# Optimization experiments

Hardware: AMD Instinct MI355X
Metric: run time of the kernel (lower is better)

Reference implementation:

```python
import jax, jax.numpy as jnp
import numpy as np

VOCAB = 6; C_IN = 4; D = 256; L = 4; T = 4096; B = 2
EXPAND = 2; DI = EXPAND * D  # 512
DS = 16; DCONV = 4; DTR = 16  # dt_rank = ceil(D/16)


def setup_inputs() -> dict:
    key = jax.random.key(0)
    ks = jax.random.split(key, 16)
    rn = lambda k, shape, s=0.02: jax.random.normal(k, shape, jnp.float32) * s
    return {
        "seq": jax.random.randint(ks[0], (B, T), 0, VOCAB),
        "input": jax.random.normal(ks[1], (B, T, C_IN), jnp.float32),
        "emb_table": rn(ks[2], (VOCAB, D)),
        "inproj_w": rn(ks[3], (D, C_IN)),
        "inproj_b": jnp.zeros((D,), jnp.float32),
        "blk_in_w": rn(ks[4], (L, 2 * DI, D)),
        "blk_in_b": jnp.zeros((L, 2 * DI), jnp.float32),
        "conv_w": rn(ks[5], (L, DI, DCONV), 0.1),
        "conv_b": jnp.zeros((L, DI), jnp.float32),
        "xproj_w": rn(ks[6], (L, DTR + 2 * DS, DI)),
        "dt_w": rn(ks[7], (L, DI, DTR), 0.1),
        "dt_b": rn(ks[8], (L, DI), 0.1),
        "A_log": jnp.log(jnp.broadcast_to(jnp.arange(1, DS + 1, dtype=jnp.float32), (L, DI, DS))),
        "Dp": jnp.ones((L, DI), jnp.float32),
        "blk_out_w": rn(ks[9], (L, D, DI)),
        "blk_out_b": jnp.zeros((L, D), jnp.float32),
        "ln_g": jnp.ones((L, D), jnp.float32),
        "ln_b": jnp.zeros((L, D), jnp.float32),
        "head_w": rn(ks[10], (VOCAB, D)),
        "head_b": jnp.zeros((VOCAB,), jnp.float32),
        "outp_w": rn(ks[11], (C_IN, D)),
        "outp_b": jnp.zeros((C_IN,), jnp.float32),
    }


def _layernorm(x, g, b):
    mu = x.mean(-1, keepdims=True)
    var = ((x - mu) ** 2).mean(-1, keepdims=True)
    return (x - mu) * jax.lax.rsqrt(var + 1e-5) * g + b


def _mamba(x, in_w, in_b, cw, cb, xpw, dtw, dtb, alog, dparam, ow, ob):
    # x: (B, T, D). Standard mamba-ssm Mamba block (d_state=DS, d_conv=DCONV, expand=2).
    Bsz = x.shape[0]
    xz = x @ in_w.T + in_b                      # (B, T, 2*DI)
    xs, z = jnp.split(xz, 2, axis=-1)           # each (B, T, DI)
    # causal depthwise conv1d over time
    xt = jnp.pad(xs.transpose(0, 2, 1), ((0, 0), (0, 0), (DCONV - 1, 0)))  # (B, DI, T+3)
    xc = jax.lax.conv_general_dilated(xt, cw[:, None, :], (1,), 'VALID',
                                      feature_group_count=DI)             # (B, DI, T)
    xc = jax.nn.silu(xc + cb[None, :, None]).transpose(0, 2, 1)           # (B, T, DI)
    # input-dependent dt, B, C
    x_dbl = xc @ xpw.T                          # (B, T, DTR+2*DS)
    dt, Bm, Cm = jnp.split(x_dbl, [DTR, DTR + DS], axis=-1)
    dt = jax.nn.softplus(dt @ dtw.T + dtb)      # (B, T, DI)
    A = -jnp.exp(alog)                          # (DI, DS)
    dA = jnp.exp(dt[..., None] * A)                                  # (B, T, DI, DS)
    dBx = dt[..., None] * Bm[:, :, None, :] * xc[..., None]          # (B, T, DI, DS)

    def step(h, ins):
        dA_t, dBx_t, C_t = ins                  # (B,DI,DS), (B,DI,DS), (B,DS)
        h = dA_t * h + dBx_t
        return h, jnp.einsum('bds,bs->bd', h, C_t)

    h0 = jnp.zeros((Bsz, DI, DS), xc.dtype)
    _, ys = jax.lax.scan(step, h0, (dA.transpose(1, 0, 2, 3),
                                    dBx.transpose(1, 0, 2, 3),
                                    Cm.transpose(1, 0, 2)))
    y = ys.transpose(1, 0, 2) + dparam * xc     # (B, T, DI)
    y = y * jax.nn.silu(z)
    return y @ ow.T + ob                        # (B, T, D)


def reference(seq, input, emb_table, inproj_w, inproj_b, blk_in_w, blk_in_b,
              conv_w, conv_b, xproj_w, dt_w, dt_b, A_log, Dp,
              blk_out_w, blk_out_b, ln_g, ln_b, head_w, head_b, outp_w, outp_b):
    x = emb_table[seq] + input @ inproj_w.T + inproj_b   # (B, T, D)
    for l in range(L):
        mx = _mamba(x, blk_in_w[l], blk_in_b[l], conv_w[l], conv_b[l],
                    xproj_w[l], dt_w[l], dt_b[l], A_log[l], Dp[l],
                    blk_out_w[l], blk_out_b[l])
        x = _layernorm(x + mx, ln_g[l], ln_b[l])
    return (x @ head_w.T + head_b, x @ outp_w.T + outp_b)
```

## Files before the change

### kernel.cpp

```cpp
#include <hip/hip_runtime.h>

typedef unsigned short u16;
typedef unsigned int u32;
typedef short bf16x8 __attribute__((ext_vector_type(8)));
typedef float f32x4 __attribute__((ext_vector_type(4)));

#define Tlen 4096
#define NTOK 8192
#define NCH  128
#define CH   32

enum : int {
  OFF_EMB     = 16,
  OFF_INPUT   = OFF_EMB + 1536,
  OFF_INPROJW = OFF_INPUT + 32768,
  OFF_INPROJB = OFF_INPROJW + 1024,
  OFF_BLKINW  = OFF_INPROJB + 256,
  OFF_BLKINB  = OFF_BLKINW + 1048576,
  OFF_CONVW   = OFF_BLKINB + 4096,
  OFF_CONVB   = OFF_CONVW + 8192,
  OFF_XPROJW  = OFF_CONVB + 2048,
  OFF_DTW     = OFF_XPROJW + 98304,
  OFF_DTB     = OFF_DTW + 32768,
  OFF_A       = OFF_DTB + 2048,
  OFF_DP      = OFF_A + 32768,
  OFF_BLKOUTW = OFF_DP + 2048,
  OFF_BLKOUTB = OFF_BLKOUTW + 524288,
  OFF_LNG     = OFF_BLKOUTB + 1024,
  OFF_LNB     = OFF_LNG + 1024,
  OFF_HEADW   = OFF_LNB + 1024,
  OFF_HEADB   = OFF_HEADW + 1536,
  OFF_OUTPW   = OFF_HEADB + 16,
  OFF_OUTPB   = OFF_OUTPW + 1024,
  OFF_X       = OFF_OUTPB + 16,
  OFF_DT      = OFF_X + NTOK*256,
  OFF_SD      = OFF_DT + NTOK*512,
  OFF_BM      = OFF_SD + 131072,
  OFF_CM      = OFF_BM + 131072,
  OFF_XSBL    = OFF_CM + 131072,
  OFF_Z16     = OFF_XSBL + NTOK*256,
  OFF_XC16    = OFF_Z16 + NTOK*256,
  OFF_X16     = OFF_XC16 + NTOK*256,
  OFF_WIN16   = OFF_X16 + NTOK*128,
  OFF_WOUT16  = OFF_WIN16 + 524288,
  OFF_BXD16   = OFF_WOUT16 + 262144,
  OFF_T       = OFF_BXD16 + 49152,
  OFF_TOT     = OFF_T + 131072,
};

__device__ inline float bf2f(u16 u) { return __uint_as_float(((u32)u) << 16); }
__device__ inline u16 f2bf(float f) {
  u32 x = __float_as_uint(f);
  u32 r = x + 0x7fffu + ((x >> 16) & 1u);
  return (u16)(r >> 16);
}

__global__ void k_sentinel(u32* dout, int nw) {
  int i = blockIdx.x * blockDim.x + threadIdx.x;
  if (i < nw) dout[i] = 0x46404640u;
}

__global__ void k_detect(const u16* emb, int n, int* flag) {
  __shared__ int bad;
  if (threadIdx.x == 0) bad = 0;
  __syncthreads();
  int local = 0;
  for (int i = threadIdx.x; i < n; i += blockDim.x) {
    float v = bf2f(emb[i]);
    if (!(fabsf(v) < 100.0f)) local = 1;
  }
  if (local) atomicOr(&bad, 1);
  __syncthreads();
  if (threadIdx.x == 0) flag[0] = bad ? 0 : 1;
}

struct Seg { const void* src; int n; int off; int op; };
struct ConvArgs { Seg seg[21]; int nseg; };

__global__ void k_convert(ConvArgs a, float* ws, const int* flag) {
  int isb = *flag;
  for (int sgi = 0; sgi < a.nseg; sgi++) {
    Seg sg = a.seg[sgi];
    for (int i = blockIdx.x * blockDim.x + threadIdx.x; i < sg.n;
         i += gridDim.x * blockDim.x) {
      float v;
      if (isb) v = bf2f(((const u16*)sg.src)[i]);
      else     v = ((const float*)sg.src)[i];
      if (sg.op) v = -__expf(v);
      ws[sg.off + i] = v;
    }
  }
}

__global__ void k_w16(float* ws) {
  u16* win = (u16*)(ws + OFF_WIN16);
  u16* wout = (u16*)(ws + OFF_WOUT16);
  for (int i = blockIdx.x * blockDim.x + threadIdx.x; i < 1048576 + 524288;
       i += gridDim.x * blockDim.x) {
    if (i < 1048576) win[i] = f2bf(ws[OFF_BLKINW + i]);
    else             wout[i - 1048576] = f2bf(ws[OFF_BLKOUTW + i - 1048576]);
  }
}

__global__ void k_bxd(float* ws) {
  u16* bxd = (u16*)(ws + OFF_BXD16);
  const int NXD = 4 * 48 * 512;
  for (int idx = blockIdx.x * blockDim.x + threadIdx.x; idx < NXD;
       idx += gridDim.x * blockDim.x) {
    int l = idx / (48 * 512);
    int rem = idx - l * (48 * 512);
    int row = rem >> 9, k = rem & 511;
    const float* xpw = ws + OFF_XPROJW + l * 24576;
    float v = (row < 32) ? xpw[(16 + row) * 512 + k] : xpw[(row - 32) * 512 + k];
    bxd[idx] = f2bf(v);
  }
}

__global__ __launch_bounds__(256) void k_embed(const int* seq, float* ws) {
  int n = blockIdx.x, d = threadIdx.x;
  int s = seq[n];
  float4 iv = *(const float4*)(ws + OFF_INPUT + n * 4);
  float4 wv = *(const float4*)(ws + OFF_INPROJW + d * 4);
  float acc = ws[OFF_EMB + s * 256 + d] + ws[OFF_INPROJB + d]
            + iv.x * wv.x + iv.y * wv.y + iv.z * wv.z + iv.w * wv.w;
  ws[OFF_X + (size_t)n * 256 + d] = acc;
  ((u16*)(ws + OFF_X16))[(size_t)n * 256 + d] = f2bf(acc);
}

__global__ __launch_bounds__(256) void k_gemm_in(float* ws, int l) {
  __shared__ u16 As[128][40];
  __shared__ u16 Bs[128][40];
  __shared__ u16 ot[64][136];
  int m0 = blockIdx.x * 128, n0g = blockIdx.y * 128;
  int t = threadIdx.x;
  int w = t >> 6, lane = t & 63;
  int fr = lane & 15, fq = lane >> 4;
  int wr = (w >> 1) * 64, wc = (w & 1) * 64;
  const u16* Ab = (const u16*)(ws + OFF_X16);
  const u16* Bb = (const u16*)(ws + OFF_WIN16) + (size_t)l * 1024 * 256;
  const float* bias = ws + OFF_BLKINB + l * 1024;
  f32x4 acc[4][4] = {};
  for (int k0 = 0; k0 < 256; k0 += 32) {
    __syncthreads();
    #pragma unroll
    for (int cc = 0; cc < 2; cc++) {
      int c = t + cc * 256;
      int row = c >> 2, cg = (c & 3) * 8;
      *(uint4*)&As[row][cg] =
          *(const uint4*)(Ab + (size_t)(m0 + row) * 256 + k0 + cg);
      *(uint4*)&Bs[row][cg] =
          *(const uint4*)(Bb + (size_t)(n0g + row) * 256 + k0 + cg);
    }
    __syncthreads();
    bf16x8 af[4], bf_[4];
    #pragma unroll
    for (int f = 0; f < 4; f++) {
      af[f]  = *(const bf16x8*)&As[wr + f * 16 + fr][fq * 8];
      bf_[f] = *(const bf16x8*)&Bs[wc + f * 16 + fr][fq * 8];
    }
    #pragma unroll
    for (int i = 0; i < 4; i++)
      #pragma unroll
      for (int j = 0; j < 4; j++)
        acc[i][j] = __builtin_amdgcn_mfma_f32_16x16x32_bf16(af[i], bf_[j],
                                                            acc[i][j], 0, 0, 0);
  }
  u16* plane; int cb0;
  if (n0g < 512) { plane = (u16*)(ws + OFF_XSBL); cb0 = n0g; }
  else           { plane = (u16*)(ws + OFF_Z16);  cb0 = n0g - 512; }
  #pragma unroll
  for (int hh = 0; hh < 2; hh++) {
    __syncthreads();
    if ((w >> 1) == hh) {
      #pragma unroll
      for (int i = 0; i < 4; i++)
        #pragma unroll
        for (int j = 0; j < 4; j++) {
          int col = wc + j * 16 + fr;
          float bv = bias[n0g + col];
          #pragma unroll
          for (int r = 0; r < 4; r++)
            ot[i * 16 + fq * 4 + r][col] = f2bf(acc[i][j][r] + bv);
        }
    }
    __syncthreads();
    int row = t >> 2, c0 = (t & 3) * 32;
    uint4 q0 = *(const uint4*)&ot[row][c0];
    uint4 q1 = *(const uint4*)&ot[row][c0 + 8];
    uint4 q2 = *(const uint4*)&ot[row][c0 + 16];
    uint4 q3 = *(const uint4*)&ot[row][c0 + 24];
    u16* dst = plane + (size_t)(m0 + hh * 64 + row) * 512 + cb0 + c0;
    *(uint4*)(dst + 0) = q0;
    *(uint4*)(dst + 8) = q1;
    *(uint4*)(dst + 16) = q2;
    *(uint4*)(dst + 24) = q3;
  }
}

__global__ __launch_bounds__(512) void k_conv(float* ws, int l) {
  int n0 = blockIdx.x * 16;
  int d = threadIdx.x;
  const float* cw = ws + OFF_CONVW + l * 2048;
  float4 w4 = *(const float4*)(cw + d * 4);
  float cbv = ws[OFF_CONVB + l * 512 + d];
  const u16* xs16 = (const u16*)(ws + OFF_XSBL);
  u16* xc16 = (u16*)(ws + OFF_XC16);
  float xm3, xm2, xm1;
  if ((n0 & (Tlen - 1)) == 0) {
    xm3 = xm2 = xm1 = 0.f;
  } else {
    xm3 = bf2f(xs16[(size_t)(n0 - 3) * 512 + d]);
    xm2 = bf2f(xs16[(size_t)(n0 - 2) * 512 + d]);
    xm1 = bf2f(xs16[(size_t)(n0 - 1) * 512 + d]);
  }
  #pragma unroll
  for (int tok = 0; tok < 16; tok++) {
    int n = n0 + tok;
    float xc = bf2f(xs16[(size_t)n * 512 + d]);
    float acc = cbv + xm3 * w4.x + xm2 * w4.y + xm1 * w4.z + xc * w4.w;
    float sv = acc / (1.f + __expf(-acc));
    xc16[(size_t)n * 512 + d] = f2bf(sv);
    xm3 = xm2; xm2 = xm1; xm1 = xc;
  }
}

__global__ __launch_bounds__(256) void k_gemm_bct(float* ws, int l) {
  int m0 = blockIdx.x * 64;
  int w = threadIdx.x >> 6, lane = threadIdx.x & 63;
  const u16* Ab = (const u16*)(ws + OFF_XC16);
  const u16* Bb = (const u16*)(ws + OFF_BXD16) + (size_t)l * 48 * 512;
  int ak = (lane >> 4) * 8;
  const u16* ap = Ab + (size_t)(m0 + w * 16 + (lane & 15)) * 512 + ak;
  int rowbase = w * 16 + (lane >> 4) * 4;
  const u16* bp = Bb + (size_t)(lane & 15) * 512 + ak;
  f32x4 acc[3] = {};
  bf16x8 a0 = *(const bf16x8*)ap;
  bf16x8 b0[3];
  #pragma unroll
  for (int j = 0; j < 3; j++) b0[j] = *(const bf16x8*)(bp + (size_t)j * 8192);
  #pragma unroll 2
  for (int k0 = 1; k0 < 16; k0++) {
    bf16x8 a1 = *(const bf16x8*)(ap + k0 * 32);
    bf16x8 b1[3];
    #pragma unroll
    for (int j = 0; j < 3; j++)
      b1[j] = *(const bf16x8*)(bp + (size_t)j * 8192 + k0 * 32);
    #pragma unroll
    for (int j = 0; j < 3; j++)
      acc[j] = __builtin_amdgcn_mfma_f32_16x16x32_bf16(a0, b0[j], acc[j], 0, 0, 0);
    a0 = a1;
    #pragma unroll
    for (int j = 0; j < 3; j++) b0[j] = b1[j];
  }
  #pragma unroll
  for (int j = 0; j < 3; j++)
    acc[j] = __builtin_amdgcn_mfma_f32_16x16x32_bf16(a0, b0[j], acc[j], 0, 0, 0);
  int c = lane & 15;
  #pragma unroll
  for (int r = 0; r < 4; r++) {
    ws[OFF_BM + (size_t)(m0 + rowbase + r) * 16 + c] = acc[0][r];
    ws[OFF_CM + (size_t)(m0 + rowbase + r) * 16 + c] = acc[1][r];
    ws[OFF_T  + (size_t)(m0 + rowbase + r) * 16 + c] = acc[2][r];
  }
}

__global__ __launch_bounds__(256) void k_dtexp(float* ws, int l) {
  __shared__ float Ts[16][16];
  int n0 = blockIdx.x * 16;
  int t = threadIdx.x;
  Ts[t >> 4][t & 15] = ws[OFF_T + (size_t)n0 * 16 + t];
  const float* dtwp = ws + OFF_DTW + (size_t)l * 8192;
  float w0[16], w1[16];
  #pragma unroll
  for (int q = 0; q < 4; q++) {
    *(float4*)&w0[q * 4] = *(const float4*)(dtwp + (2 * t) * 16 + q * 4);
    *(float4*)&w1[q * 4] = *(const float4*)(dtwp + (2 * t + 1) * 16 + q * 4);
  }
  float b0 = ws[OFF_DTB + l * 512 + 2 * t];
  float b1 = ws[OFF_DTB + l * 512 + 2 * t + 1];
  __syncthreads();
  u16* dt16 = (u16*)(ws + OFF_DT);
  #pragma unroll
  for (int tok = 0; tok < 16; tok++) {
    float s0 = b0, s1 = b1;
    #pragma unroll
    for (int r = 0; r < 16; r++) {
      float tv = Ts[tok][r];
      s0 += tv * w0[r];
      s1 += tv * w1[r];
    }
    float d0 = (s0 > 20.f) ? s0 : log1pf(__expf(s0));
    float d1 = (s1 > 20.f) ? s1 : log1pf(__expf(s1));
    *(u32*)(dt16 + (size_t)(n0 + tok) * 512 + 2 * t) =
        (u32)f2bf(d0) | ((u32)f2bf(d1) << 16);
  }
}

__global__ __launch_bounds__(512) void k_scan1(float* ws, int l) {
  __shared__ u16 dt_s[8][512];
  __shared__ u16 xc_s[8][512];
  __shared__ float Bls[CH * 16];
  int blk = blockIdx.x;
  int b = blk >> 7, ch = blk & 127;
  int d = threadIdx.x;
  int nbase = b * Tlen + ch * CH;
  Bls[d] = ws[OFF_BM + (size_t)nbase * 16 + d];
  const float* Ap = ws + OFF_A + l * 8192 + d * 16;
  float Ar[16];
  *(float4*)&Ar[0]  = *(const float4*)(Ap + 0);
  *(float4*)&Ar[4]  = *(const float4*)(Ap + 4);
  *(float4*)&Ar[8]  = *(const float4*)(Ap + 8);
  *(float4*)&Ar[12] = *(const float4*)(Ap + 12);
  float h[16];
  #pragma unroll
  for (int s = 0; s < 16; s++) h[s] = 0.f;
  float sumdt = 0.f;
  const u16* dtg = (const u16*)(ws + OFF_DT) + (size_t)nbase * 512;
  const u16* xcg = (const u16*)(ws + OFF_XC16) + (size_t)nbase * 512;
  int lr = d >> 6, lc = (d & 63) * 8;
  uint4 pd = *(const uint4*)(dtg + (size_t)lr * 512 + lc);
  uint4 px = *(const uint4*)(xcg + (size_t)lr * 512 + lc);
  for (int st = 0; st < 4; st++) {
    *(uint4*)&dt_s[lr][lc] = pd;
    *(uint4*)&xc_s[lr][lc] = px;
    if (st < 3) {
      pd = *(const uint4*)(dtg + (size_t)(st * 8 + 8 + lr) * 512 + lc);
      px = *(const uint4*)(xcg + (size_t)(st * 8 + 8 + lr) * 512 + lc);
    }
    __syncthreads();
    #pragma unroll
    for (int tk = 0; tk < 8; tk++) {
      int tt = st * 8 + tk;
      float dtv = bf2f(dt_s[tk][d]);
      float xv = bf2f(xc_s[tk][d]);
      sumdt += dtv;
      float dtx = dtv * xv;
      #pragma unroll
      for (int s = 0; s < 16; s++)
        h[s] = __expf(dtv * Ar[s]) * h[s] + dtx * Bls[tt * 16 + s];
    }
    __syncthreads();
  }
  ws[OFF_SD + (size_t)blk * 512 + d] = sumdt;
  float* bl = ws + OFF_XSBL + ((size_t)blk * 512 + d) * 16;
  *(float4*)(bl + 0)  = make_float4(h[0], h[1], h[2], h[3]);
  *(float4*)(bl + 4)  = make_float4(h[4], h[5], h[6], h[7]);
  *(float4*)(bl + 8)  = make_float4(h[8], h[9], h[10], h[11]);
  *(float4*)(bl + 12) = make_float4(h[12], h[13], h[14], h[15]);
}

__global__ __launch_bounds__(256) void k_scan2(float* ws, int l) {
  int q = blockIdx.x * 256 + threadIdx.x;
  int b = q >> 13, ds = q & 8191, d = ds >> 4;
  float Av = ws[OFF_A + l * 8192 + ds];
  float* blhs = ws + OFF_XSBL;
  const float* sdp = ws + OFF_SD;
  size_t base = (size_t)(b * NCH) * 8192 + ds;
  size_t sbase = (size_t)(b * NCH) * 512 + d;
  float blv[4], sd[4];
  #pragma unroll
  for (int k = 0; k < 4; k++) {
    blv[k] = blhs[base + (size_t)k * 8192];
    sd[k] = sdp[sbase + (size_t)k * 512];
  }
  float h = 0.f;
  for (int g = 0; g < 32; g++) {
    float nblv[4], nsd[4];
    if (g < 31) {
      #pragma unroll
      for (int k = 0; k < 4; k++) {
        nblv[k] = blhs[base + (size_t)(g * 4 + 4 + k) * 8192];
        nsd[k] = sdp[sbase + (size_t)(g * 4 + 4 + k) * 512];
      }
    }
    #pragma unroll
    for (int k = 0; k < 4; k++) {
      blhs[base + (size_t)(g * 4 + k) * 8192] = h;
      h = __expf(sd[k] * Av) * h + blv[k];
    }
    #pragma unroll
    for (int k = 0; k < 4; k++) { blv[k] = nblv[k]; sd[k] = nsd[k]; }
  }
}

__global__ __launch_bounds__(512) void k_scan3(float* ws, int l) {
  __shared__ u16 dt_s[8][512];
  __shared__ u16 xc_s[8][512];
  __shared__ u16 z_s[8][512];
  __shared__ u16 y_s[8][512];
  __shared__ float Bls[CH * 16];
  __shared__ float Cls[CH * 16];
  int blk = blockIdx.x;
  int b = blk >> 7, ch = blk & 127;
  int d = threadIdx.x;
  int nbase = b * Tlen + ch * CH;
  Bls[d] = ws[OFF_BM + (size_t)nbase * 16 + d];
  Cls[d] = ws[OFF_CM + (size_t)nbase * 16 + d];
  const float* Ap = ws + OFF_A + l * 8192 + d * 16;
  float Ar[16];
  *(float4*)&Ar[0]  = *(const float4*)(Ap + 0);
  *(float4*)&Ar[4]  = *(const float4*)(Ap + 4);
  *(float4*)&Ar[8]  = *(const float4*)(Ap + 8);
  *(float4*)&Ar[12] = *(const float4*)(Ap + 12);
  float Dv = ws[OFF_DP + l * 512 + d];
  const float* hs = ws + OFF_XSBL + ((size_t)blk * 512 + d) * 16;
  float h[16];
  *(float4*)&h[0]  = *(const float4*)(hs + 0);
  *(float4*)&h[4]  = *(const float4*)(hs + 4);
  *(float4*)&h[8]  = *(const float4*)(hs + 8);
  *(float4*)&h[12] = *(const float4*)(hs + 12);
  const u16* dtg = (const u16*)(ws + OFF_DT) + (size_t)nbase * 512;
  u16* xcg = (u16*)(ws + OFF_XC16) + (size_t)nbase * 512;
  const u16* zg = (const u16*)(ws + OFF_Z16) + (size_t)nbase * 512;
  int lr = d >> 6, lc = (d & 63) * 8;
  size_t off0 = (size_t)lr * 512 + lc;
  uint4 pd = *(const uint4*)(dtg + off0);
  uint4 px = *(const uint4*)(xcg + off0);
  uint4 pz = *(const uint4*)(zg + off0);
  for (int st = 0; st < 4; st++) {
    size_t goff = (size_t)(st * 8 + lr) * 512 + lc;
    *(uint4*)&dt_s[lr][lc] = pd;
    *(uint4*)&xc_s[lr][lc] = px;
    *(uint4*)&z_s[lr][lc]  = pz;
    if (st < 3) {
      size_t noff = (size_t)(st * 8 + 8 + lr) * 512 + lc;
      pd = *(const uint4*)(dtg + noff);
      px = *(const uint4*)(xcg + noff);
      pz = *(const uint4*)(zg + noff);
    }
    __syncthreads();
    #pragma unroll
    for (int tk = 0; tk < 8; tk++) {
      int tt = st * 8 + tk;
      float dtv = bf2f(dt_s[tk][d]);
      float xv = bf2f(xc_s[tk][d]);
      float dtx = dtv * xv;
      float yacc = 0.f;
      #pragma unroll
      for (int s = 0; s < 16; s++) {
        h[s] = __expf(dtv * Ar[s]) * h[s] + dtx * Bls[tt * 16 + s];
        yacc += h[s] * Cls[tt * 16 + s];
      }
      float yv = yacc + Dv * xv;
      float zv = bf2f(z_s[tk][d]);
      float sz = zv / (1.f + __expf(-zv));
      y_s[tk][d] = f2bf(yv * sz);
    }
    __syncthreads();
    *(uint4*)(xcg + goff) = *(const uint4*)&y_s[lr][lc];
  }
}

__global__ __launch_bounds__(256) void k_gemm_out(float* ws, int l) {
  __shared__ float mxs[16][260];
  int m0 = blockIdx.x * 16;
  int w = threadIdx.x >> 6, lane = threadIdx.x & 63;
  const u16* Ab = (const u16*)(ws + OFF_XC16);
  const u16* Bb = (const u16*)(ws + OFF_WOUT16) + (size_t)l * 256 * 512;
  int ak = (lane >> 4) * 8;
  const u16* ap = Ab + (size_t)(m0 + (lane & 15)) * 512 + ak;
  const u16* bp = Bb + (size_t)(w * 64 + (lane & 15)) * 512 + ak;
  f32x4 acc[4] = {};
  bf16x8 a0 = *(const bf16x8*)ap;
  bf16x8 b0[4];
  #pragma unroll
  for (int j = 0; j < 4; j++) b0[j] = *(const bf16x8*)(bp + (size_t)j * 8192);
  #pragma unroll 2
  for (int k0 = 1; k0 < 16; k0++) {
    bf16x8 a1 = *(const bf16x8*)(ap + k0 * 32);
    bf16x8 b1[4];
    #pragma unroll
    for (int j = 0; j < 4; j++)
      b1[j] = *(const bf16x8*)(bp + (size_t)j * 8192 + k0 * 32);
    #pragma unroll
    for (int j = 0; j < 4; j++)
      acc[j] = __builtin_amdgcn_mfma_f32_16x16x32_bf16(a0, b0[j], acc[j], 0, 0, 0);
    a0 = a1;
    #pragma unroll
    for (int j = 0; j < 4; j++) b0[j] = b1[j];
  }
  #pragma unroll
  for (int j = 0; j < 4; j++)
    acc[j] = __builtin_amdgcn_mfma_f32_16x16x32_bf16(a0, b0[j], acc[j], 0, 0, 0);
  const float* ob = ws + OFF_BLKOUTB + l * 256;
  int rl = (lane >> 4) * 4;
  #pragma unroll
  for (int j = 0; j < 4; j++) {
    int c = w * 64 + j * 16 + (lane & 15);
    float bv = ob[c];
    #pragma unroll
    for (int r = 0; r < 4; r++)
      mxs[rl + r][c] = acc[j][r] + bv;
  }
  __syncthreads();
  int t = threadIdx.x;
  int g = t >> 4, ln = t & 15;
  int n = m0 + g;
  float* x = ws + OFF_X;
  const float* gamma = ws + OFF_LNG + l * 256;
  const float* beta = ws + OFF_LNB + l * 256;
  float v[16], s1 = 0.f, s2 = 0.f;
  #pragma unroll
  for (int i = 0; i < 16; i++) {
    int c = ln + i * 16;
    float xv = x[(size_t)n * 256 + c] + mxs[g][c];
    v[i] = xv; s1 += xv; s2 += xv * xv;
  }
  #pragma unroll
  for (int m = 8; m >= 1; m >>= 1) {
    s1 += __shfl_xor(s1, m, 64);
    s2 += __shfl_xor(s2, m, 64);
  }
  float mu = s1 * (1.f / 256.f);
  float var = s2 * (1.f / 256.f) - mu * mu;
  float rs = rsqrtf(var + 1e-5f);
  #pragma unroll
  for (int i = 0; i < 16; i++) {
    int c = ln + i * 16;
    mxs[g][c] = (v[i] - mu) * rs * gamma[c] + beta[c];
  }
  __syncthreads();
  int row = t >> 4, cb = (t & 15) * 16;
  float4 f0 = *(const float4*)&mxs[row][cb + 0];
  float4 f1 = *(const float4*)&mxs[row][cb + 4];
  float4 f2 = *(const float4*)&mxs[row][cb + 8];
  float4 f3 = *(const float4*)&mxs[row][cb + 12];
  float* xd = x + (size_t)(m0 + row) * 256 + cb;
  *(float4*)(xd + 0) = f0;
  *(float4*)(xd + 4) = f1;
  *(float4*)(xd + 8) = f2;
  *(float4*)(xd + 12) = f3;
  u32 p[8];
  p[0] = (u32)f2bf(f0.x) | ((u32)f2bf(f0.y) << 16);
  p[1] = (u32)f2bf(f0.z) | ((u32)f2bf(f0.w) << 16);
  p[2] = (u32)f2bf(f1.x) | ((u32)f2bf(f1.y) << 16);
  p[3] = (u32)f2bf(f1.z) | ((u32)f2bf(f1.w) << 16);
  p[4] = (u32)f2bf(f2.x) | ((u32)f2bf(f2.y) << 16);
  p[5] = (u32)f2bf(f2.z) | ((u32)f2bf(f2.w) << 16);
  p[6] = (u32)f2bf(f3.x) | ((u32)f2bf(f3.y) << 16);
  p[7] = (u32)f2bf(f3.z) | ((u32)f2bf(f3.w) << 16);
  u16* xd16 = (u16*)(ws + OFF_X16) + (size_t)(m0 + row) * 256 + cb;
  *(uint4*)(xd16 + 0) = *(uint4*)&p[0];
  *(uint4*)(xd16 + 8) = *(uint4*)&p[4];
}

__global__ __launch_bounds__(256) void k_head(const float* ws, void* dout,
                                              const int* flag) {
  int t = threadIdx.x;
  int lane = t & 63, w = t >> 6;
  int n = blockIdx.x * 4 + w;
  const float* xr = ws + OFF_X + (size_t)n * 256;
  float xv[4];
  #pragma unroll
  for (int i = 0; i < 4; i++) xv[i] = xr[lane + 64 * i];
  float res[10];
  #pragma unroll
  for (int o = 0; o < 10; o++) {
    const float* wr = (o < 6) ? ws + OFF_HEADW + o * 256
                              : ws + OFF_OUTPW + (o - 6) * 256;
    float p = 0.f;
    #pragma unroll
    for (int i = 0; i < 4; i++) p += xv[i] * wr[lane + 64 * i];
    #pragma unroll
    for (int m = 32; m >= 1; m >>= 1) p += __shfl_xor(p, m, 64);
    res[o] = p;
  }
  int isb = flag[0];
  if (lane < 6) {
    float vv = res[lane] + ws[OFF_HEADB + lane];
    size_t idx = (size_t)n * 6 + lane;
    if (isb) ((u16*)dout)[idx] = f2bf(vv);
    else     ((float*)dout)[idx] = vv;
  } else if (lane < 10) {
    int o = lane - 6;
    float vv = res[lane] + ws[OFF_OUTPB + o];
    size_t idx = (size_t)NTOK * 6 + (size_t)n * 4 + o;
    if (isb) ((u16*)dout)[idx] = f2bf(vv);
    else     ((float*)dout)[idx] = vv;
  }
}

extern "C" void kernel_launch(void* const* d_in, const int* in_sizes, int n_in,
                              void* d_out, int out_size, void* d_ws, size_t ws_size,
                              hipStream_t stream) {
  (void)n_in;
  float* ws = (float*)d_ws;
  int* flag = (int*)d_ws;

  if (ws_size < (size_t)OFF_TOT * 4) {
    int nw = out_size / 2;
    k_sentinel<<<(nw + 255) / 256, 256, 0, stream>>>((u32*)d_out, nw);
    return;
  }

  k_detect<<<1, 256, 0, stream>>>((const u16*)d_in[2], in_sizes[2], flag);

  ConvArgs ca;
  int i = 0;
  auto add = [&](int idx, int n, int off, int op) {
    ca.seg[i].src = d_in[idx]; ca.seg[i].n = n;
    ca.seg[i].off = off; ca.seg[i].op = op; i++;
  };
  add(2, 1536, OFF_EMB, 0);      add(1, 32768, OFF_INPUT, 0);
  add(3, 1024, OFF_INPROJW, 0);  add(4, 256, OFF_INPROJB, 0);
  add(5, 1048576, OFF_BLKINW, 0); add(6, 4096, OFF_BLKINB, 0);
  add(7, 8192, OFF_CONVW, 0);    add(8, 2048, OFF_CONVB, 0);
  add(9, 98304, OFF_XPROJW, 0);  add(10, 32768, OFF_DTW, 0);
  add(11, 2048, OFF_DTB, 0);     add(12, 32768, OFF_A, 1);
  add(13, 2048, OFF_DP, 0);      add(14, 524288, OFF_BLKOUTW, 0);
  add(15, 1024, OFF_BLKOUTB, 0); add(16, 1024, OFF_LNG, 0);
  add(17, 1024, OFF_LNB, 0);     add(18, 1536, OFF_HEADW, 0);
  add(19, 6, OFF_HEADB, 0);      add(20, 1024, OFF_OUTPW, 0);
  add(21, 4, OFF_OUTPB, 0);
  ca.nseg = i;
  k_convert<<<512, 256, 0, stream>>>(ca, ws, flag);
  k_w16<<<512, 256, 0, stream>>>(ws);
  k_bxd<<<384, 256, 0, stream>>>(ws);

  k_embed<<<NTOK, 256, 0, stream>>>((const int*)d_in[0], ws);

  for (int l = 0; l < 4; l++) {
    k_gemm_in<<<dim3(64, 8), 256, 0, stream>>>(ws, l);
    k_conv<<<NTOK / 16, 512, 0, stream>>>(ws, l);
    k_gemm_bct<<<128, 256, 0, stream>>>(ws, l);
    k_dtexp<<<NTOK / 16, 256, 0, stream>>>(ws, l);
    k_scan1<<<2 * NCH, 512, 0, stream>>>(ws, l);
    k_scan2<<<64, 256, 0, stream>>>(ws, l);
    k_scan3<<<2 * NCH, 512, 0, stream>>>(ws, l);
    k_gemm_out<<<NTOK / 16, 256, 0, stream>>>(ws, l);
  }

  k_head<<<NTOK / 4, 256, 0, stream>>>(ws, d_out, flag);
}
```

Baseline: 562.2 us.

## Fuse dt projection and softplus into scan kernels, drop dtexp kernel

Removes the separate k_dtexp kernel and its bf16 dt buffer; both scan1 and scan3 now recompute dt per token from the low-rank T vector (staged in shared memory) and per-channel dt weights held in registers, then apply softplus. This eliminates a kernel launch plus a write and two reads of an 8192x512 bf16 tensor per layer, in exchange for doing the 16-term dot product and log1p/exp twice on the serial scan path and holding 16 more registers per thread. It also keeps dt in fp32 rather than rounding it to bf16.

```diff
diff --git a/kernel.cpp b/kernel.cpp
--- a/kernel.cpp
+++ b/kernel.cpp
@@ -33,8 +33,7 @@
   OFF_OUTPW   = OFF_HEADB + 16,
   OFF_OUTPB   = OFF_OUTPW + 1024,
   OFF_X       = OFF_OUTPB + 16,
-  OFF_DT      = OFF_X + NTOK*256,
-  OFF_SD      = OFF_DT + NTOK*512,
+  OFF_SD      = OFF_X + NTOK*256,
   OFF_BM      = OFF_SD + 131072,
   OFF_CM      = OFF_BM + 131072,
   OFF_XSBL    = OFF_CM + 131072,
@@ -264,74 +263,48 @@
   }
 }
 
-__global__ __launch_bounds__(256) void k_dtexp(float* ws, int l) {
-  __shared__ float Ts[16][16];
-  int n0 = blockIdx.x * 16;
-  int t = threadIdx.x;
-  Ts[t >> 4][t & 15] = ws[OFF_T + (size_t)n0 * 16 + t];
-  const float* dtwp = ws + OFF_DTW + (size_t)l * 8192;
-  float w0[16], w1[16];
-  #pragma unroll
-  for (int q = 0; q < 4; q++) {
-    *(float4*)&w0[q * 4] = *(const float4*)(dtwp + (2 * t) * 16 + q * 4);
-    *(float4*)&w1[q * 4] = *(const float4*)(dtwp + (2 * t + 1) * 16 + q * 4);
-  }
-  float b0 = ws[OFF_DTB + l * 512 + 2 * t];
-  float b1 = ws[OFF_DTB + l * 512 + 2 * t + 1];
-  __syncthreads();
-  u16* dt16 = (u16*)(ws + OFF_DT);
-  #pragma unroll
-  for (int tok = 0; tok < 16; tok++) {
-    float s0 = b0, s1 = b1;
-    #pragma unroll
-    for (int r = 0; r < 16; r++) {
-      float tv = Ts[tok][r];
-      s0 += tv * w0[r];
-      s1 += tv * w1[r];
-    }
-    float d0 = (s0 > 20.f) ? s0 : log1pf(__expf(s0));
-    float d1 = (s1 > 20.f) ? s1 : log1pf(__expf(s1));
-    *(u32*)(dt16 + (size_t)(n0 + tok) * 512 + 2 * t) =
-        (u32)f2bf(d0) | ((u32)f2bf(d1) << 16);
-  }
-}
-
 __global__ __launch_bounds__(512) void k_scan1(float* ws, int l) {
-  __shared__ u16 dt_s[8][512];
   __shared__ u16 xc_s[8][512];
+  __shared__ float T_s[CH * 16];
   __shared__ float Bls[CH * 16];
   int blk = blockIdx.x;
   int b = blk >> 7, ch = blk & 127;
   int d = threadIdx.x;
   int nbase = b * Tlen + ch * CH;
   Bls[d] = ws[OFF_BM + (size_t)nbase * 16 + d];
+  T_s[d] = ws[OFF_T + (size_t)nbase * 16 + d];
   const float* Ap = ws + OFF_A + l * 8192 + d * 16;
   float Ar[16];
   *(float4*)&Ar[0]  = *(const float4*)(Ap + 0);
   *(float4*)&Ar[4]  = *(const float4*)(Ap + 4);
   *(float4*)&Ar[8]  = *(const float4*)(Ap + 8);
   *(float4*)&Ar[12] = *(const float4*)(Ap + 12);
+  const float* dtwp = ws + OFF_DTW + (size_t)l * 8192 + d * 16;
+  float wd[16];
+  *(float4*)&wd[0]  = *(const float4*)(dtwp + 0);
+  *(float4*)&wd[4]  = *(const float4*)(dtwp + 4);
+  *(float4*)&wd[8]  = *(const float4*)(dtwp + 8);
+  *(float4*)&wd[12] = *(const float4*)(dtwp + 12);
+  float bd = ws[OFF_DTB + l * 512 + d];
   float h[16];
   #pragma unroll
   for (int s = 0; s < 16; s++) h[s] = 0.f;
   float sumdt = 0.f;
-  const u16* dtg = (const u16*)(ws + OFF_DT) + (size_t)nbase * 512;
   const u16* xcg = (const u16*)(ws + OFF_XC16) + (size_t)nbase * 512;
   int lr = d >> 6, lc = (d & 63) * 8;
-  uint4 pd = *(const uint4*)(dtg + (size_t)lr * 512 + lc);
   uint4 px = *(const uint4*)(xcg + (size_t)lr * 512 + lc);
   for (int st = 0; st < 4; st++) {
-    *(uint4*)&dt_s[lr][lc] = pd;
     *(uint4*)&xc_s[lr][lc] = px;
-    if (st < 3) {
-      pd = *(const uint4*)(dtg + (size_t)(st * 8 + 8 + lr) * 512 + lc);
+    if (st < 3)
       px = *(const uint4*)(xcg + (size_t)(st * 8 + 8 + lr) * 512 + lc);
-    }
     __syncthreads();
     #pragma unroll
     for (int tk = 0; tk < 8; tk++) {
       int tt = st * 8 + tk;
-      float dtv = bf2f(dt_s[tk][d]);
+      float s0 = bd;
+      #pragma unroll
+      for (int r = 0; r < 16; r++) s0 += T_s[tt * 16 + r] * wd[r];
+      float dtv = (s0 > 20.f) ? s0 : log1pf(__expf(s0));
       float xv = bf2f(xc_s[tk][d]);
       sumdt += dtv;
       float dtx = dtv * xv;
@@ -384,10 +357,10 @@
 }
 
 __global__ __launch_bounds__(512) void k_scan3(float* ws, int l) {
-  __shared__ u16 dt_s[8][512];
   __shared__ u16 xc_s[8][512];
   __shared__ u16 z_s[8][512];
   __shared__ u16 y_s[8][512];
+  __shared__ float T_s[CH * 16];
   __shared__ float Bls[CH * 16];
   __shared__ float Cls[CH * 16];
   int blk = blockIdx.x;
@@ -396,12 +369,20 @@
   int nbase = b * Tlen + ch * CH;
   Bls[d] = ws[OFF_BM + (size_t)nbase * 16 + d];
   Cls[d] = ws[OFF_CM + (size_t)nbase * 16 + d];
+  T_s[d] = ws[OFF_T + (size_t)nbase * 16 + d];
   const float* Ap = ws + OFF_A + l * 8192 + d * 16;
   float Ar[16];
   *(float4*)&Ar[0]  = *(const float4*)(Ap + 0);
   *(float4*)&Ar[4]  = *(const float4*)(Ap + 4);
   *(float4*)&Ar[8]  = *(const float4*)(Ap + 8);
   *(float4*)&Ar[12] = *(const float4*)(Ap + 12);
+  const float* dtwp = ws + OFF_DTW + (size_t)l * 8192 + d * 16;
+  float wd[16];
+  *(float4*)&wd[0]  = *(const float4*)(dtwp + 0);
+  *(float4*)&wd[4]  = *(const float4*)(dtwp + 4);
+  *(float4*)&wd[8]  = *(const float4*)(dtwp + 8);
+  *(float4*)&wd[12] = *(const float4*)(dtwp + 12);
+  float bd = ws[OFF_DTB + l * 512 + d];
   float Dv = ws[OFF_DP + l * 512 + d];
   const float* hs = ws + OFF_XSBL + ((size_t)blk * 512 + d) * 16;
   float h[16];
@@ -409,22 +390,18 @@
   *(float4*)&h[4]  = *(const float4*)(hs + 4);
   *(float4*)&h[8]  = *(const float4*)(hs + 8);
   *(float4*)&h[12] = *(const float4*)(hs + 12);
-  const u16* dtg = (const u16*)(ws + OFF_DT) + (size_t)nbase * 512;
   u16* xcg = (u16*)(ws + OFF_XC16) + (size_t)nbase * 512;
   const u16* zg = (const u16*)(ws + OFF_Z16) + (size_t)nbase * 512;
   int lr = d >> 6, lc = (d & 63) * 8;
   size_t off0 = (size_t)lr * 512 + lc;
-  uint4 pd = *(const uint4*)(dtg + off0);
   uint4 px = *(const uint4*)(xcg + off0);
   uint4 pz = *(const uint4*)(zg + off0);
   for (int st = 0; st < 4; st++) {
     size_t goff = (size_t)(st * 8 + lr) * 512 + lc;
-    *(uint4*)&dt_s[lr][lc] = pd;
     *(uint4*)&xc_s[lr][lc] = px;
     *(uint4*)&z_s[lr][lc]  = pz;
     if (st < 3) {
       size_t noff = (size_t)(st * 8 + 8 + lr) * 512 + lc;
-      pd = *(const uint4*)(dtg + noff);
       px = *(const uint4*)(xcg + noff);
       pz = *(const uint4*)(zg + noff);
     }
@@ -432,7 +409,10 @@
     #pragma unroll
     for (int tk = 0; tk < 8; tk++) {
       int tt = st * 8 + tk;
-      float dtv = bf2f(dt_s[tk][d]);
+      float s0 = bd;
+      #pragma unroll
+      for (int r = 0; r < 16; r++) s0 += T_s[tt * 16 + r] * wd[r];
+      float dtv = (s0 > 20.f) ? s0 : log1pf(__expf(s0));
       float xv = bf2f(xc_s[tk][d]);
       float dtx = dtv * xv;
       float yacc = 0.f;
@@ -623,7 +603,6 @@
     k_gemm_in<<<dim3(64, 8), 256, 0, stream>>>(ws, l);
     k_conv<<<NTOK / 16, 512, 0, stream>>>(ws, l);
     k_gemm_bct<<<128, 256, 0, stream>>>(ws, l);
-    k_dtexp<<<NTOK / 16, 256, 0, stream>>>(ws, l);
     k_scan1<<<2 * NCH, 512, 0, stream>>>(ws, l);
     k_scan2<<<64, 256, 0, stream>>>(ws, l);
     k_scan3<<<2 * NCH, 512, 0, stream>>>(ws, l);
```

Result: slower. 615.6 us (+9.5%).
